# Kernel tuning notes

Hardware: AMD Instinct MI355X
Metric: run time of the kernel (lower is better)

Reference implementation:

```python
import jax, jax.numpy as jnp
import numpy as np
import math

B, S, D, H_HEADS, K_SPAN = 2, 2048, 64, 12, 512  # batch, seq, head dim, heads, pos_ebd_size


def setup_inputs() -> dict:
    key = jax.random.key(0)
    ks = jax.random.split(key, 12)
    init = lambda k, shp: (jax.random.normal(k, shp, dtype=jnp.float32) * 0.02)
    H = jax.random.normal(ks[0], (B, S, D), dtype=jnp.float32)
    pos_embeddings = jax.random.normal(ks[1], (2 * K_SPAN, D), dtype=jnp.float32)
    # classic DeBERTa relative positions: i - j (2-D, as required by the torch code path)
    idx = jnp.arange(S)
    relative_pos = (idx[:, None] - idx[None, :]).astype(jnp.int64)
    OH = H_HEADS * D
    return {
        "H": H,
        "pos_embeddings": pos_embeddings,
        "relative_pos": relative_pos,
        "Wq": init(ks[2], (OH, D)), "bq": jnp.zeros((OH,), jnp.float32),
        "Wk": init(ks[3], (OH, D)), "bk": jnp.zeros((OH,), jnp.float32),
        "Wv": init(ks[4], (OH, D)), "bv": jnp.zeros((OH,), jnp.float32),
        "Wpq": init(ks[5], (OH, D)), "bpq": jnp.zeros((OH,), jnp.float32),
        "Wpk": init(ks[6], (OH, D)), "bpk": jnp.zeros((OH,), jnp.float32),
    }


def _heads(x):
    # [..., S, h*d] -> [..., h, S, d]
    b, s, _ = x.shape
    return x.reshape(b, s, H_HEADS, D).transpose(0, 2, 1, 3)


def reference(H, pos_embeddings, relative_pos, Wq, bq, Wk, bk, Wv, bv, Wpq, bpq, Wpk, bpk):
    proj = lambda x, W, b: x @ W.T + b
    q = _heads(proj(H, Wq, bq))  # [B,h,S,d]
    k = _heads(proj(H, Wk, bk))
    v = _heads(proj(H, Wv, bv))

    # content-to-content scores
    scores = jnp.einsum('bhqd,bhkd->bhqk', q, k)  # [B,h,S,S]

    # relative position projections over the full 2K span
    pk = proj(pos_embeddings, Wpk, bpk).reshape(2 * K_SPAN, H_HEADS, D).transpose(1, 0, 2)  # [h,2K,d]
    pq = proj(pos_embeddings, Wpq, bpq).reshape(2 * K_SPAN, H_HEADS, D).transpose(1, 0, 2)

    rel = relative_pos.astype(jnp.int32)
    # content-to-position: gather over 2K axis with clamped (i-j)+K
    c2p = jnp.einsum('bhqd,hrd->bhqr', q, pk)  # [B,h,S,2K]
    c2p_pos = jnp.clip(rel + K_SPAN, 0, 2 * K_SPAN - 1)  # [S,S]
    c2p_idx = jnp.broadcast_to(c2p_pos[None, None], (B, H_HEADS, S, S))
    c2p_att = jnp.take_along_axis(c2p, c2p_idx, axis=-1)  # [B,h,S,S]

    # position-to-content: gather over 2K axis with clamped -(i-j)+K, then transpose
    p2c = jnp.einsum('bhkd,hrd->bhkr', k, pq)  # [B,h,S,2K]
    p2c_pos = jnp.clip(-rel + K_SPAN, 0, 2 * K_SPAN - 1)
    p2c_idx = jnp.broadcast_to(p2c_pos[None, None], (B, H_HEADS, S, S))
    p2c_att = jnp.take_along_axis(p2c, p2c_idx, axis=-1).swapaxes(-1, -2)  # [B,h,S,S]

    scores = (scores + c2p_att + p2c_att) / math.sqrt(D * 3)
    probs = jax.nn.softmax(scores, axis=-1)
    ctx = jnp.einsum('bhqk,bhkd->bhqd', probs, v)  # [B,h,S,d]
    return ctx.transpose(0, 2, 1, 3).reshape(B, S, H_HEADS * D)
```

## Files before the change

### kernel.cpp

```cpp
#include <hip/hip_runtime.h>
#include <math.h>


#define S_LEN 2048
#define NH    12
#define TWOK  1024
#define QSZ   3145728
#define PSZ   786432
#define POSF  11010048

typedef __bf16 bf16x8 __attribute__((ext_vector_type(8)));
typedef unsigned short u16x8 __attribute__((ext_vector_type(8)));
typedef float f32x4  __attribute__((ext_vector_type(4)));
typedef float f32x16 __attribute__((ext_vector_type(16)));
typedef unsigned int u32x2 __attribute__((ext_vector_type(2)));
typedef unsigned int u32x4 __attribute__((ext_vector_type(4)));

__device__ __forceinline__ unsigned short f2bf(float f) {
  return __builtin_bit_cast(unsigned short, (__bf16)f);
}
__device__ __forceinline__ unsigned pk2bf(float a, float b) {
  return ((unsigned)__builtin_bit_cast(unsigned short, (__bf16)b) << 16)
       | (unsigned)__builtin_bit_cast(unsigned short, (__bf16)a);
}
__device__ __forceinline__ float bf2f(unsigned short h) {
  return __builtin_bit_cast(float, ((unsigned)h) << 16);
}
__device__ __forceinline__ bf16x8 ld_bf8(const unsigned short* p) {
  return __builtin_bit_cast(bf16x8, *(const u16x8*)p);
}

__global__ __launch_bounds__(256) void prep_kernel(
    const float* __restrict__ Hx, const float* __restrict__ pos,
    const float* __restrict__ Wq, const float* __restrict__ Wk,
    const float* __restrict__ Wv, const float* __restrict__ Wpk,
    const float* __restrict__ Wpq,
    const float* __restrict__ bq, const float* __restrict__ bk,
    const float* __restrict__ bv, const float* __restrict__ bpk,
    const float* __restrict__ bpq,
    unsigned short* __restrict__ whi, unsigned short* __restrict__ wlo,
    unsigned short* __restrict__ wall, float* __restrict__ ball) {
  int idx = blockIdx.x * 256 + threadIdx.x;
  if (idx < 327680) {
    float v = (idx < 262144) ? Hx[idx] : pos[idx - 262144];
    __bf16 hi = (__bf16)v;
    float lo = v - (float)hi;
    whi[idx] = __builtin_bit_cast(unsigned short, hi);
    wlo[idx] = f2bf(lo);
  } else if (idx < 573440) {
    int k = idx - 327680;
    int mat = k / 49152, off = k - mat * 49152;
    const float* W = mat==0?Wq: mat==1?Wk: mat==2?Wv: mat==3?Wpk:Wpq;
    wall[k] = f2bf(W[off]);
  } else if (idx < 577280) {
    int k = idx - 573440;
    int mat = k / 768, off = k - mat * 768;
    const float* B = mat==0?bq: mat==1?bk: mat==2?bv: mat==3?bpk:bpq;
    ball[k] = B[off];
  }
}

__global__ __launch_bounds__(256) void proj_gemm(
    const unsigned short* __restrict__ whi, const unsigned short* __restrict__ wlo,
    const unsigned short* __restrict__ wall, const float* __restrict__ ball,
    unsigned short* __restrict__ ws) {
  unsigned short* qg  = ws;
  unsigned short* kg  = ws + QSZ;
  unsigned short* vtg = ws + 2 * QSZ;
  unsigned short* pkg = ws + 3 * QSZ;
  unsigned short* pqg = ws + 3 * QSZ + PSZ;

  int bid = blockIdx.x;
  int rbase, obase, wrow, isA;
  if (bid < 2304) { rbase = (bid / 36) * 64;        obase = (bid % 36) * 64; wrow = obase;        isA = 1; }
  else { int b2 = bid - 2304; rbase = 4096 + (b2 / 24) * 64; obase = (b2 % 24) * 64; wrow = 2304 + obase; isA = 0; }

  int tid = threadIdx.x, w = tid >> 6, l = tid & 63, lg = l >> 4, lr = l & 15;
  int xrow = rbase + w * 16 + lr;

  bf16x8 ah[2], al[2];
  #pragma unroll
  for (int ks = 0; ks < 2; ++ks) {
    ah[ks] = ld_bf8(whi + xrow * 64 + ks * 32 + 8 * lg);
    al[ks] = ld_bf8(wlo + xrow * 64 + ks * 32 + 8 * lg);
  }

  int mat = obase / 768;
  int h = ((obase % 768) >> 6);

  #pragma unroll
  for (int jb = 0; jb < 4; ++jb) {
    f32x4 acc = {0.f, 0.f, 0.f, 0.f};
    #pragma unroll
    for (int ks = 0; ks < 2; ++ks) {
      bf16x8 bfrag = ld_bf8(wall + (wrow + jb * 16 + lr) * 64 + ks * 32 + 8 * lg);
      acc = __builtin_amdgcn_mfma_f32_16x16x32_bf16(ah[ks], bfrag, acc, 0, 0, 0);
      acc = __builtin_amdgcn_mfma_f32_16x16x32_bf16(al[ks], bfrag, acc, 0, 0, 0);
    }
    float bias = ball[wrow + jb * 16 + lr];
    int d = jb * 16 + lr;
    #pragma unroll
    for (int r = 0; r < 4; ++r) {
      int orow = rbase + w * 16 + 4 * lg + r;
      unsigned short val = f2bf(acc[r] + bias);
      if (isA) {
        int bb = orow >> 11, i = orow & 2047, bh = bb * NH + h;
        if (mat == 0)      qg[(bh * S_LEN + i) * 64 + d] = val;
        else if (mat == 1) kg[(bh * S_LEN + i) * 64 + d] = val;
        else               vtg[(bh * 64 + d) * S_LEN + i] = val;
      } else {
        int prow = orow - 4096;
        if (mat == 0) pkg[(h * TWOK + prow) * 64 + d] = val;
        else          pqg[(h * TWOK + prow) * 64 + d] = val;
      }
    }
  }
}

__global__ __launch_bounds__(256) void pos_dots(
    const unsigned short* __restrict__ ws, float* __restrict__ c2p0,
    float* __restrict__ c2p1023, float* __restrict__ p2c0,
    float* __restrict__ p2c1023) {
  int t = blockIdx.x * 256 + threadIdx.x;
  int isK = t >= 49152;
  int row = isK ? t - 49152 : t;
  int h = (row >> 11) % NH;
  const unsigned short* src = ws + (isK ? QSZ : 0) + row * 64;
  const unsigned short* pA = ws + 3 * QSZ + (isK ? PSZ : 0) + (h * TWOK) * 64;
  const unsigned short* pB = pA + 1023 * 64;
  float a0 = 0.f, a1 = 0.f;
  #pragma unroll
  for (int c = 0; c < 8; ++c) {
    u16x8 xv = *(const u16x8*)(src + c * 8);
    u16x8 av = *(const u16x8*)(pA + c * 8);
    u16x8 bv = *(const u16x8*)(pB + c * 8);
    #pragma unroll
    for (int e = 0; e < 8; ++e) {
      float x = bf2f(xv[e]);
      a0 += x * bf2f(av[e]);
      a1 += x * bf2f(bv[e]);
    }
  }
  if (isK) { p2c0[row] = a0; p2c1023[row] = a1; }
  else     { c2p0[row] = a0; c2p1023[row] = a1; }
}

__global__ __launch_bounds__(64, 2) void attn_kernel(
    const unsigned short* __restrict__ ws, float* __restrict__ out) {
  const unsigned short* qg  = ws;
  const unsigned short* kg  = ws + QSZ;
  const unsigned short* vtg = ws + 2 * QSZ;
  const unsigned short* pkg = ws + 3 * QSZ;
  const unsigned short* pqg = ws + 3 * QSZ + PSZ;
  const float* c2p0g    = (const float*)(ws + POSF);
  const float* c2p1023g = c2p0g + 49152;
  const float* p2c0g    = c2p0g + 98304;
  const float* p2c1023g = c2p0g + 147456;

  __shared__ __align__(16) unsigned short tblC[96 * 32];
  __shared__ __align__(16) unsigned short tblP[64 * 128];

  const int bid = blockIdx.x;
  const int g = bid & 7, r = bid >> 3;
  const int bh = 8 * (r % 3) + g;
  const int it32 = r / 3;
  const int b = bh / NH, h = bh - b * NH;
  const int l = threadIdx.x & 63;
  const int iL = l & 31, h5 = l >> 5;
  const int i0w = it32 * 32;
  const int ig = i0w + iL;

  const unsigned short* qb  = qg  + bh * (S_LEN * 64);
  const unsigned short* kb  = kg  + bh * (S_LEN * 64);
  const unsigned short* vb  = vtg + bh * (64 * S_LEN);
  const unsigned short* pkb = pkg + h * (TWOK * 64);
  const unsigned short* pqb = pqg + h * (TWOK * 64);

  const float CS = 1.4426950408889634f / sqrtf(192.0f);

  bf16x8 qf[4];
  #pragma unroll
  for (int kc = 0; kc < 4; ++kc)
    qf[kc] = ld_bf8(qb + ig * 64 + kc * 16 + 8 * h5);

  const float c2pLO = c2p0g[bh * S_LEN + ig];
  const float c2pHI = c2p1023g[bh * S_LEN + ig];

  f32x16 ctx0 = 0.f, ctx1 = 0.f;
  float m_ = -1e30f, l_ = 0.f;

  char* tPw = (char*)tblP;
  char* pb0 = tPw + iL * 256;
  char* pb1 = tPw + (32 + iL) * 256;
  const int wxor = (iL & 15) << 4;

  for (int jt = 0; jt < 32; ++jt) {
    const int j0 = jt * 64;
    const int rlo = 512 + i0w - j0 - 63;
    const int rhi = rlo + 94;

    bf16x8 kf0[4], kf1[4];
    #pragma unroll
    for (int kc = 0; kc < 4; ++kc) {
      kf0[kc] = ld_bf8(kb + (j0 + iL) * 64 + kc * 16 + 8 * h5);
      kf1[kc] = ld_bf8(kb + (j0 + 32 + iL) * 64 + kc * 16 + 8 * h5);
    }
    bf16x8 vf0[4], vf1[4];
    #pragma unroll
    for (int kc = 0; kc < 4; ++kc) {
      vf0[kc] = ld_bf8(vb + (iL) * S_LEN + j0 + kc * 16 + 8 * h5);
      vf1[kc] = ld_bf8(vb + (32 + iL) * S_LEN + j0 + kc * 16 + 8 * h5);
    }

    f32x16 s0 = 0.f, s1 = 0.f;
    #pragma unroll
    for (int kc = 0; kc < 4; ++kc) {
      s0 = __builtin_amdgcn_mfma_f32_32x32x16_bf16(kf0[kc], qf[kc], s0, 0, 0, 0);
      s1 = __builtin_amdgcn_mfma_f32_32x32x16_bf16(kf1[kc], qf[kc], s1, 0, 0, 0);
    }

    if (rlo >= 1023) {
      float pa = p2c1023g[bh * S_LEN + j0 + iL];
      float pb = p2c1023g[bh * S_LEN + j0 + 32 + iL];
      #pragma unroll
      for (int r = 0; r < 16; ++r) {
        const int j32 = (r & 3) + 8 * (r >> 2) + 4 * h5;
        s0[r] = (s0[r] + c2pHI + __shfl(pa, j32)) * CS;
        s1[r] = (s1[r] + c2pHI + __shfl(pb, j32)) * CS;
      }
    } else if (rhi <= 0) {
      float pa = p2c0g[bh * S_LEN + j0 + iL];
      float pb = p2c0g[bh * S_LEN + j0 + 32 + iL];
      #pragma unroll
      for (int r = 0; r < 16; ++r) {
        const int j32 = (r & 3) + 8 * (r >> 2) + 4 * h5;
        s0[r] = (s0[r] + c2pLO + __shfl(pa, j32)) * CS;
        s1[r] = (s1[r] + c2pLO + __shfl(pb, j32)) * CS;
      }
    } else {
      const int rminc = rlo < 0 ? 0 : rlo;
      const int rmaxc = rhi > 1023 ? 1023 : rhi;
      const int bstart = rminc > 928 ? 928 : rminc;
      const int nbh = (rmaxc - bstart) >> 5;
      const int interior = (rlo >= 0) & (rhi <= 1023);
      int c_lo = (rminc - bstart) >> 5;
      int p0_lo, p1_hi;
      if (interior) {
        p0_lo = (rlo + 32 - bstart) >> 5;
        p1_hi = (rhi - 32 - bstart) >> 5;
      } else { p0_lo = c_lo; p1_hi = nbh; }

      for (int nb = c_lo; nb <= nbh; ++nb) {
        const int rrow = bstart + nb * 32 + iL;
        const int doP0 = nb >= p0_lo, doP1 = nb <= p1_hi;
        f32x16 ac = 0.f, a0 = 0.f, a1 = 0.f;
        #pragma unroll
        for (int kc = 0; kc < 4; ++kc) {
          bf16x8 fk = ld_bf8(pkb + rrow * 64 + kc * 16 + 8 * h5);
          ac = __builtin_amdgcn_mfma_f32_32x32x16_bf16(fk, qf[kc], ac, 0, 0, 0);
        }
        if (doP0 | doP1) {
          #pragma unroll
          for (int kc = 0; kc < 4; ++kc) {
            bf16x8 fq = ld_bf8(pqb + rrow * 64 + kc * 16 + 8 * h5);
            if (doP0) a0 = __builtin_amdgcn_mfma_f32_32x32x16_bf16(fq, kf0[kc], a0, 0, 0, 0);
            if (doP1) a1 = __builtin_amdgcn_mfma_f32_32x32x16_bf16(fq, kf1[kc], a1, 0, 0, 0);
          }
        }
        #pragma unroll
        for (int q4 = 0; q4 < 4; ++q4) {
          const int Rq = nb * 32 + 8 * q4 + 4 * h5;
          #pragma unroll
          for (int e = 0; e < 4; ++e)
            tblC[(Rq + e) * 32 + iL] = f2bf(ac[4 * q4 + e]);
        }
        #pragma unroll
        for (int q4 = 0; q4 < 4; ++q4) {
          const int off = ((nb * 32 + 8 * q4 + 4 * h5) * 2) ^ wxor;
          if (doP0) {
            u32x2 v0; v0[0] = pk2bf(a0[4*q4+0], a0[4*q4+1]); v0[1] = pk2bf(a0[4*q4+2], a0[4*q4+3]);
            *(u32x2*)(pb0 + off) = v0;
          }
          if (doP1) {
            u32x2 v1; v1[0] = pk2bf(a1[4*q4+0], a1[4*q4+1]); v1[1] = pk2bf(a1[4*q4+2], a1[4*q4+3]);
            *(u32x2*)(pb1 + off) = v1;
          }
        }
      }
      asm volatile("s_waitcnt lgkmcnt(0)" ::: "memory");

      const int D0 = ig + 512 - j0;
      if (interior) {
        const int rb0 = D0 - bstart;
        #pragma unroll
        for (int r = 0; r < 16; ++r) {
          const int j32 = (r & 3) + 8 * (r >> 2) + 4 * h5;
          const int pxr = (j32 & 15) << 4;
          const int o0 = (rb0 - j32) * 2, o1 = o0 - 64;
          float c0v = bf2f(tblC[(rb0 - j32) * 32 + iL]);
          float c1v = bf2f(tblC[(rb0 - 32 - j32) * 32 + iL]);
          float p0v = bf2f(*(const unsigned short*)(tPw + j32 * 256 + (o0 ^ pxr)));
          float p1v = bf2f(*(const unsigned short*)(tPw + (32 + j32) * 256 + (o1 ^ pxr)));
          s0[r] = (s0[r] + c0v + p0v) * CS;
          s1[r] = (s1[r] + c1v + p1v) * CS;
        }
      } else {
        #pragma unroll
        for (int r = 0; r < 16; ++r) {
          const int j32 = (r & 3) + 8 * (r >> 2) + 4 * h5;
          const int pxr = (j32 & 15) << 4;
          int rel0 = D0 - j32;       rel0 = rel0 < 0 ? 0 : (rel0 > 1023 ? 1023 : rel0);
          int rel1 = D0 - 32 - j32;  rel1 = rel1 < 0 ? 0 : (rel1 > 1023 ? 1023 : rel1);
          const int rb0 = rel0 - bstart, rb1 = rel1 - bstart;
          float c0v = bf2f(tblC[rb0 * 32 + iL]);
          float c1v = bf2f(tblC[rb1 * 32 + iL]);
          float p0v = bf2f(*(const unsigned short*)(tPw + j32 * 256 + ((rb0 * 2) ^ pxr)));
          float p1v = bf2f(*(const unsigned short*)(tPw + (32 + j32) * 256 + ((rb1 * 2) ^ pxr)));
          s0[r] = (s0[r] + c0v + p0v) * CS;
          s1[r] = (s1[r] + c1v + p1v) * CS;
        }
      }
    }

    float vmax = s0[0];
    #pragma unroll
    for (int r = 1; r < 16; ++r) vmax = fmaxf(vmax, s0[r]);
    #pragma unroll
    for (int r = 0; r < 16; ++r) vmax = fmaxf(vmax, s1[r]);
    vmax = fmaxf(vmax, __shfl_xor(vmax, 32));
    float mx = fmaxf(m_, vmax);
    float fs = __builtin_amdgcn_exp2f(m_ - mx);
    m_ = mx;
    float sum = 0.f;
    #pragma unroll
    for (int r = 0; r < 16; ++r) { s0[r] = __builtin_amdgcn_exp2f(s0[r] - mx); sum += s0[r]; }
    #pragma unroll
    for (int r = 0; r < 16; ++r) { s1[r] = __builtin_amdgcn_exp2f(s1[r] - mx); sum += s1[r]; }
    sum += __shfl_xor(sum, 32);
    l_ = l_ * fs + sum;
    if (!__all(fs == 1.0f)) { ctx0 *= fs; ctx1 *= fs; }

    bf16x8 pf[4];
    #pragma unroll
    for (int kc = 0; kc < 4; ++kc) {
      const int c = kc & 1;
      const f32x16& sj = (kc >> 1) ? s1 : s0;
      unsigned X0 = pk2bf(sj[8*c+0], sj[8*c+1]);
      unsigned X1 = pk2bf(sj[8*c+2], sj[8*c+3]);
      unsigned Y0 = pk2bf(sj[8*c+4], sj[8*c+5]);
      unsigned Y1 = pk2bf(sj[8*c+6], sj[8*c+7]);
      unsigned sx0 = (unsigned)__shfl_xor((int)X0, 32);
      unsigned sx1 = (unsigned)__shfl_xor((int)X1, 32);
      unsigned sy0 = (unsigned)__shfl_xor((int)Y0, 32);
      unsigned sy1 = (unsigned)__shfl_xor((int)Y1, 32);
      u32x4 f;
      f[0] = h5 ? sy0 : X0;
      f[1] = h5 ? sy1 : X1;
      f[2] = h5 ? Y0 : sx0;
      f[3] = h5 ? Y1 : sx1;
      pf[kc] = __builtin_bit_cast(bf16x8, f);
    }

    #pragma unroll
    for (int kc = 0; kc < 4; ++kc) {
      ctx0 = __builtin_amdgcn_mfma_f32_32x32x16_bf16(vf0[kc], pf[kc], ctx0, 0, 0, 0);
      ctx1 = __builtin_amdgcn_mfma_f32_32x32x16_bf16(vf1[kc], pf[kc], ctx1, 0, 0, 0);
    }
  }

  float inv = 1.0f / l_;
  float* ob = out + (b * S_LEN + ig) * 768 + h * 64;
  #pragma unroll
  for (int q4 = 0; q4 < 4; ++q4) {
    float4 o0 = {ctx0[4*q4+0]*inv, ctx0[4*q4+1]*inv, ctx0[4*q4+2]*inv, ctx0[4*q4+3]*inv};
    *(float4*)(ob + 8 * q4 + 4 * h5) = o0;
    float4 o1 = {ctx1[4*q4+0]*inv, ctx1[4*q4+1]*inv, ctx1[4*q4+2]*inv, ctx1[4*q4+3]*inv};
    *(float4*)(ob + 32 + 8 * q4 + 4 * h5) = o1;
  }
}

extern "C" void kernel_launch(void* const* d_in, const int* in_sizes, int n_in,
                              void* d_out, int out_size, void* d_ws, size_t ws_size,
                              hipStream_t stream) {
  (void)in_sizes; (void)n_in; (void)out_size; (void)ws_size;
  const float* Hx  = (const float*)d_in[0];
  const float* pos = (const float*)d_in[1];
  const float* Wq  = (const float*)d_in[3];  const float* bq  = (const float*)d_in[4];
  const float* Wk  = (const float*)d_in[5];  const float* bk  = (const float*)d_in[6];
  const float* Wv  = (const float*)d_in[7];  const float* bv  = (const float*)d_in[8];
  const float* Wpq = (const float*)d_in[9];  const float* bpq = (const float*)d_in[10];
  const float* Wpk = (const float*)d_in[11]; const float* bpk = (const float*)d_in[12];
  unsigned short* ws = (unsigned short*)d_ws;

  unsigned short* scratch = (unsigned short*)d_out;
  unsigned short* whi  = scratch;
  unsigned short* wlo  = scratch + 327680;
  unsigned short* wall = scratch + 655360;
  float*          ball = (float*)(scratch + 901120);

  float* c2p0g    = (float*)(ws + POSF);
  float* c2p1023g = c2p0g + 49152;
  float* p2c0g    = c2p0g + 98304;
  float* p2c1023g = c2p0g + 147456;

  prep_kernel<<<2255, 256, 0, stream>>>(Hx, pos, Wq, Wk, Wv, Wpk, Wpq,
                                        bq, bk, bv, bpk, bpq, whi, wlo, wall, ball);
  proj_gemm<<<2688, 256, 0, stream>>>(whi, wlo, wall, ball, ws);
  pos_dots<<<384, 256, 0, stream>>>(ws, c2p0g, c2p1023g, p2c0g, p2c1023g);
  attn_kernel<<<1536, 64, 0, stream>>>(ws, (float*)d_out);
}
```

Measured before the change: 334.4 us.

## Split attention over key blocks, skip unused position bands, vectorize projection stores

The attention kernel gains a split-K (flash-decoding style) mode. Each query tile's key range is split into up to 4 chunks that run as separate blocks and write bf16 partial context plus (m, l). A new combine kernel merges them. The position-band loop now computes only the c2p/p2c bands that actually fall in the tile's diagonal window, and writes them into one packed LDS table. The projection GEMM is re-oriented so outputs are stored as 4-wide vectors instead of scalar 2-byte stores, and launch bounds raise occupancy to 4 waves. The split depends on the workspace size, adds an extra kernel and partial-buffer traffic, and stores partial context in bf16, which costs some precision.

```diff
diff --git a/kernel.cpp b/kernel.cpp
--- a/kernel.cpp
+++ b/kernel.cpp
@@ -11,9 +11,9 @@
 
 typedef __bf16 bf16x8 __attribute__((ext_vector_type(8)));
 typedef unsigned short u16x8 __attribute__((ext_vector_type(8)));
+typedef unsigned short u16x4 __attribute__((ext_vector_type(4)));
 typedef float f32x4  __attribute__((ext_vector_type(4)));
 typedef float f32x16 __attribute__((ext_vector_type(16)));
-typedef unsigned int u32x2 __attribute__((ext_vector_type(2)));
 typedef unsigned int u32x4 __attribute__((ext_vector_type(4)));
 
 __device__ __forceinline__ unsigned short f2bf(float f) {
@@ -76,42 +76,60 @@
   else { int b2 = bid - 2304; rbase = 4096 + (b2 / 24) * 64; obase = (b2 % 24) * 64; wrow = 2304 + obase; isA = 0; }
 
   int tid = threadIdx.x, w = tid >> 6, l = tid & 63, lg = l >> 4, lr = l & 15;
-  int xrow = rbase + w * 16 + lr;
-
-  bf16x8 ah[2], al[2];
+  int mat = obase / 768;
+  int h = (obase % 768) >> 6;
+  int ohrow = wrow + w * 16;
+
+  bf16x8 wf[2];
   #pragma unroll
-  for (int ks = 0; ks < 2; ++ks) {
-    ah[ks] = ld_bf8(whi + xrow * 64 + ks * 32 + 8 * lg);
-    al[ks] = ld_bf8(wlo + xrow * 64 + ks * 32 + 8 * lg);
-  }
-
-  int mat = obase / 768;
-  int h = ((obase % 768) >> 6);
-
-  #pragma unroll
-  for (int jb = 0; jb < 4; ++jb) {
-    f32x4 acc = {0.f, 0.f, 0.f, 0.f};
-    #pragma unroll
-    for (int ks = 0; ks < 2; ++ks) {
-      bf16x8 bfrag = ld_bf8(wall + (wrow + jb * 16 + lr) * 64 + ks * 32 + 8 * lg);
-      acc = __builtin_amdgcn_mfma_f32_16x16x32_bf16(ah[ks], bfrag, acc, 0, 0, 0);
-      acc = __builtin_amdgcn_mfma_f32_16x16x32_bf16(al[ks], bfrag, acc, 0, 0, 0);
-    }
-    float bias = ball[wrow + jb * 16 + lr];
-    int d = jb * 16 + lr;
-    #pragma unroll
-    for (int r = 0; r < 4; ++r) {
-      int orow = rbase + w * 16 + 4 * lg + r;
-      unsigned short val = f2bf(acc[r] + bias);
+  for (int ks = 0; ks < 2; ++ks)
+    wf[ks] = ld_bf8(wall + (ohrow + lr) * 64 + ks * 32 + 8 * lg);
+
+  if (isA && mat == 2) {
+    float bias = ball[ohrow + lr];
+    int d = w * 16 + lr;
+    #pragma unroll
+    for (int tg = 0; tg < 4; ++tg) {
+      f32x4 acc = {0.f, 0.f, 0.f, 0.f};
+      #pragma unroll
+      for (int ks = 0; ks < 2; ++ks) {
+        bf16x8 xh = ld_bf8(whi + (rbase + tg * 16 + lr) * 64 + ks * 32 + 8 * lg);
+        bf16x8 xl = ld_bf8(wlo + (rbase + tg * 16 + lr) * 64 + ks * 32 + 8 * lg);
+        acc = __builtin_amdgcn_mfma_f32_16x16x32_bf16(xh, wf[ks], acc, 0, 0, 0);
+        acc = __builtin_amdgcn_mfma_f32_16x16x32_bf16(xl, wf[ks], acc, 0, 0, 0);
+      }
+      int tok0 = rbase + tg * 16 + 4 * lg;
+      int bb = tok0 >> 11, i0 = tok0 & 2047, bh = bb * NH + h;
+      u16x4 pv;
+      #pragma unroll
+      for (int e = 0; e < 4; ++e) pv[e] = f2bf(acc[e] + bias);
+      *(u16x4*)(vtg + (size_t)(bh * 64 + d) * S_LEN + i0) = pv;
+    }
+  } else {
+    float4 bias4 = *(const float4*)(ball + ohrow + 4 * lg);
+    int d0 = w * 16 + 4 * lg;
+    #pragma unroll
+    for (int tg = 0; tg < 4; ++tg) {
+      f32x4 acc = {0.f, 0.f, 0.f, 0.f};
+      #pragma unroll
+      for (int ks = 0; ks < 2; ++ks) {
+        bf16x8 xh = ld_bf8(whi + (rbase + tg * 16 + lr) * 64 + ks * 32 + 8 * lg);
+        bf16x8 xl = ld_bf8(wlo + (rbase + tg * 16 + lr) * 64 + ks * 32 + 8 * lg);
+        acc = __builtin_amdgcn_mfma_f32_16x16x32_bf16(wf[ks], xh, acc, 0, 0, 0);
+        acc = __builtin_amdgcn_mfma_f32_16x16x32_bf16(wf[ks], xl, acc, 0, 0, 0);
+      }
+      int tok = rbase + tg * 16 + lr;
+      u16x4 pv;
+      pv[0] = f2bf(acc[0] + bias4.x); pv[1] = f2bf(acc[1] + bias4.y);
+      pv[2] = f2bf(acc[2] + bias4.z); pv[3] = f2bf(acc[3] + bias4.w);
       if (isA) {
-        int bb = orow >> 11, i = orow & 2047, bh = bb * NH + h;
-        if (mat == 0)      qg[(bh * S_LEN + i) * 64 + d] = val;
-        else if (mat == 1) kg[(bh * S_LEN + i) * 64 + d] = val;
-        else               vtg[(bh * 64 + d) * S_LEN + i] = val;
+        int bb = tok >> 11, i = tok & 2047, bh = bb * NH + h;
+        unsigned short* dst = (mat == 0 ? qg : kg) + (size_t)(bh * S_LEN + i) * 64 + d0;
+        *(u16x4*)dst = pv;
       } else {
-        int prow = orow - 4096;
-        if (mat == 0) pkg[(h * TWOK + prow) * 64 + d] = val;
-        else          pqg[(h * TWOK + prow) * 64 + d] = val;
+        int prow = tok - 4096;
+        unsigned short* dst = (mat == 0 ? pkg : pqg) + (size_t)(h * TWOK + prow) * 64 + d0;
+        *(u16x4*)dst = pv;
       }
     }
   }
@@ -145,8 +163,10 @@
   else     { c2p0[row] = a0; c2p1023[row] = a1; }
 }
 
-__global__ __launch_bounds__(64, 2) void attn_kernel(
-    const unsigned short* __restrict__ ws, float* __restrict__ out) {
+template<int SPLIT>
+__global__ __launch_bounds__(64, 4) void attn_kernel(
+    const unsigned short* __restrict__ ws, float* __restrict__ out,
+    unsigned short* __restrict__ ctxP, float* __restrict__ mlP) {
   const unsigned short* qg  = ws;
   const unsigned short* kg  = ws + QSZ;
   const unsigned short* vtg = ws + 2 * QSZ;
@@ -157,11 +177,12 @@
   const float* p2c0g    = c2p0g + 98304;
   const float* p2c1023g = c2p0g + 147456;
 
-  __shared__ __align__(16) unsigned short tblC[96 * 32];
-  __shared__ __align__(16) unsigned short tblP[64 * 128];
+  __shared__ unsigned int tbl2[64 * 32];
 
   const int bid = blockIdx.x;
-  const int g = bid & 7, r = bid >> 3;
+  const int g = bid & 7;
+  const int r2 = bid >> 3;
+  const int sk = r2 % SPLIT, r = r2 / SPLIT;
   const int bh = 8 * (r % 3) + g;
   const int it32 = r / 3;
   const int b = bh / NH, h = bh - b * NH;
@@ -189,14 +210,13 @@
   f32x16 ctx0 = 0.f, ctx1 = 0.f;
   float m_ = -1e30f, l_ = 0.f;
 
-  char* tPw = (char*)tblP;
-  char* pb0 = tPw + iL * 256;
-  char* pb1 = tPw + (32 + iL) * 256;
-  const int wxor = (iL & 15) << 4;
-
-  for (int jt = 0; jt < 32; ++jt) {
+  const int jt0 = sk * (32 / SPLIT);
+  const int jt1 = jt0 + (32 / SPLIT);
+
+  for (int jt = jt0; jt < jt1; ++jt) {
     const int j0 = jt * 64;
-    const int rlo = 512 + i0w - j0 - 63;
+    const int D0w = 512 + i0w - j0;
+    const int rlo = D0w - 63;
     const int rhi = rlo + 94;
 
     bf16x8 kf0[4], kf1[4];
@@ -223,119 +243,129 @@
       float pa = p2c1023g[bh * S_LEN + j0 + iL];
       float pb = p2c1023g[bh * S_LEN + j0 + 32 + iL];
       #pragma unroll
-      for (int r = 0; r < 16; ++r) {
-        const int j32 = (r & 3) + 8 * (r >> 2) + 4 * h5;
-        s0[r] = (s0[r] + c2pHI + __shfl(pa, j32)) * CS;
-        s1[r] = (s1[r] + c2pHI + __shfl(pb, j32)) * CS;
+      for (int rr = 0; rr < 16; ++rr) {
+        const int j32 = (rr & 3) + 8 * (rr >> 2) + 4 * h5;
+        s0[rr] = (s0[rr] + c2pHI + __shfl(pa, j32)) * CS;
+        s1[rr] = (s1[rr] + c2pHI + __shfl(pb, j32)) * CS;
       }
     } else if (rhi <= 0) {
       float pa = p2c0g[bh * S_LEN + j0 + iL];
       float pb = p2c0g[bh * S_LEN + j0 + 32 + iL];
       #pragma unroll
-      for (int r = 0; r < 16; ++r) {
-        const int j32 = (r & 3) + 8 * (r >> 2) + 4 * h5;
-        s0[r] = (s0[r] + c2pLO + __shfl(pa, j32)) * CS;
-        s1[r] = (s1[r] + c2pLO + __shfl(pb, j32)) * CS;
+      for (int rr = 0; rr < 16; ++rr) {
+        const int j32 = (rr & 3) + 8 * (rr >> 2) + 4 * h5;
+        s0[rr] = (s0[rr] + c2pLO + __shfl(pa, j32)) * CS;
+        s1[rr] = (s1[rr] + c2pLO + __shfl(pb, j32)) * CS;
       }
     } else {
       const int rminc = rlo < 0 ? 0 : rlo;
       const int rmaxc = rhi > 1023 ? 1023 : rhi;
       const int bstart = rminc > 928 ? 928 : rminc;
-      const int nbh = (rmaxc - bstart) >> 5;
+      const int nbands = ((rmaxc - bstart) >> 5) + 1;
+      const int base = D0w - bstart;
       const int interior = (rlo >= 0) & (rhi <= 1023);
-      int c_lo = (rminc - bstart) >> 5;
-      int p0_lo, p1_hi;
-      if (interior) {
-        p0_lo = (rlo + 32 - bstart) >> 5;
-        p1_hi = (rhi - 32 - bstart) >> 5;
-      } else { p0_lo = c_lo; p1_hi = nbh; }
-
-      for (int nb = c_lo; nb <= nbh; ++nb) {
-        const int rrow = bstart + nb * 32 + iL;
-        const int doP0 = nb >= p0_lo, doP1 = nb <= p1_hi;
-        f32x16 ac = 0.f, a0 = 0.f, a1 = 0.f;
-        #pragma unroll
-        for (int kc = 0; kc < 4; ++kc) {
-          bf16x8 fk = ld_bf8(pkb + rrow * 64 + kc * 16 + 8 * h5);
-          ac = __builtin_amdgcn_mfma_f32_32x32x16_bf16(fk, qf[kc], ac, 0, 0, 0);
+
+      for (int nb = 0; nb < nbands; ++nb) {
+        const int relb0 = nb * 32;
+        const bool needC  = (relb0 <= base + 31) && (relb0 + 31 >= base - 63);
+        const bool needP0 = (relb0 <= base + 31) && (relb0 + 31 >= base - 31);
+        const bool needP1 = (relb0 <= base - 1)  && (relb0 + 31 >= base - 63);
+        const int rrow = bstart + relb0 + iL;
+
+        if (needC) {
+          f32x16 ac = 0.f;
+          #pragma unroll
+          for (int kc = 0; kc < 4; ++kc) {
+            bf16x8 fk = ld_bf8(pkb + rrow * 64 + kc * 16 + 8 * h5);
+            ac = __builtin_amdgcn_mfma_f32_32x32x16_bf16(fk, qf[kc], ac, 0, 0, 0);
+          }
+          #pragma unroll
+          for (int q4 = 0; q4 < 4; ++q4) {
+            #pragma unroll
+            for (int e = 0; e < 4; ++e) {
+              const int relb = relb0 + 8 * q4 + 4 * h5 + e;
+              const int js = base + iL - relb;
+              if (js >= 0 && js < 64)
+                ((unsigned short*)tbl2)[(js * 32 + iL) * 2] = f2bf(ac[4 * q4 + e]);
+            }
+          }
         }
-        if (doP0 | doP1) {
+        if (needP0 | needP1) {
+          f32x16 a0 = 0.f, a1 = 0.f;
           #pragma unroll
           for (int kc = 0; kc < 4; ++kc) {
             bf16x8 fq = ld_bf8(pqb + rrow * 64 + kc * 16 + 8 * h5);
-            if (doP0) a0 = __builtin_amdgcn_mfma_f32_32x32x16_bf16(fq, kf0[kc], a0, 0, 0, 0);
-            if (doP1) a1 = __builtin_amdgcn_mfma_f32_32x32x16_bf16(fq, kf1[kc], a1, 0, 0, 0);
+            if (needP0) a0 = __builtin_amdgcn_mfma_f32_32x32x16_bf16(fq, kf0[kc], a0, 0, 0, 0);
+            if (needP1) a1 = __builtin_amdgcn_mfma_f32_32x32x16_bf16(fq, kf1[kc], a1, 0, 0, 0);
+          }
+          #pragma unroll
+          for (int q4 = 0; q4 < 4; ++q4) {
+            #pragma unroll
+            for (int e = 0; e < 4; ++e) {
+              const int relb = relb0 + 8 * q4 + 4 * h5 + e;
+              if (needP0) {
+                const int i2 = relb + iL - base;
+                if (i2 >= 0 && i2 < 32)
+                  ((unsigned short*)tbl2)[(iL * 32 + i2) * 2 + 1] = f2bf(a0[4 * q4 + e]);
+              }
+              if (needP1) {
+                const int i2 = relb + 32 + iL - base;
+                if (i2 >= 0 && i2 < 32)
+                  ((unsigned short*)tbl2)[((32 + iL) * 32 + i2) * 2 + 1] = f2bf(a1[4 * q4 + e]);
+              }
+            }
           }
         }
+      }
+      asm volatile("s_waitcnt lgkmcnt(0)" ::: "memory");
+
+      if (interior) {
         #pragma unroll
-        for (int q4 = 0; q4 < 4; ++q4) {
-          const int Rq = nb * 32 + 8 * q4 + 4 * h5;
-          #pragma unroll
-          for (int e = 0; e < 4; ++e)
-            tblC[(Rq + e) * 32 + iL] = f2bf(ac[4 * q4 + e]);
-        }
-        #pragma unroll
-        for (int q4 = 0; q4 < 4; ++q4) {
-          const int off = ((nb * 32 + 8 * q4 + 4 * h5) * 2) ^ wxor;
-          if (doP0) {
-            u32x2 v0; v0[0] = pk2bf(a0[4*q4+0], a0[4*q4+1]); v0[1] = pk2bf(a0[4*q4+2], a0[4*q4+3]);
-            *(u32x2*)(pb0 + off) = v0;
-          }
-          if (doP1) {
-            u32x2 v1; v1[0] = pk2bf(a1[4*q4+0], a1[4*q4+1]); v1[1] = pk2bf(a1[4*q4+2], a1[4*q4+3]);
-            *(u32x2*)(pb1 + off) = v1;
-          }
-        }
-      }
-      asm volatile("s_waitcnt lgkmcnt(0)" ::: "memory");
-
-      const int D0 = ig + 512 - j0;
-      if (interior) {
-        const int rb0 = D0 - bstart;
-        #pragma unroll
-        for (int r = 0; r < 16; ++r) {
-          const int j32 = (r & 3) + 8 * (r >> 2) + 4 * h5;
-          const int pxr = (j32 & 15) << 4;
-          const int o0 = (rb0 - j32) * 2, o1 = o0 - 64;
-          float c0v = bf2f(tblC[(rb0 - j32) * 32 + iL]);
-          float c1v = bf2f(tblC[(rb0 - 32 - j32) * 32 + iL]);
-          float p0v = bf2f(*(const unsigned short*)(tPw + j32 * 256 + (o0 ^ pxr)));
-          float p1v = bf2f(*(const unsigned short*)(tPw + (32 + j32) * 256 + (o1 ^ pxr)));
-          s0[r] = (s0[r] + c0v + p0v) * CS;
-          s1[r] = (s1[r] + c1v + p1v) * CS;
+        for (int rr = 0; rr < 16; ++rr) {
+          const int j32 = (rr & 3) + 8 * (rr >> 2) + 4 * h5;
+          const unsigned t0 = tbl2[j32 * 32 + iL];
+          const unsigned t1 = tbl2[(32 + j32) * 32 + iL];
+          s0[rr] = (s0[rr] + bf2f((unsigned short)t0) + bf2f((unsigned short)(t0 >> 16))) * CS;
+          s1[rr] = (s1[rr] + bf2f((unsigned short)t1) + bf2f((unsigned short)(t1 >> 16))) * CS;
         }
       } else {
+        const int D0 = D0w + iL;
+        float paL = p2c0g[bh * S_LEN + j0 + iL];
+        float paH = p2c1023g[bh * S_LEN + j0 + iL];
+        float pbL = p2c0g[bh * S_LEN + j0 + 32 + iL];
+        float pbH = p2c1023g[bh * S_LEN + j0 + 32 + iL];
         #pragma unroll
-        for (int r = 0; r < 16; ++r) {
-          const int j32 = (r & 3) + 8 * (r >> 2) + 4 * h5;
-          const int pxr = (j32 & 15) << 4;
-          int rel0 = D0 - j32;       rel0 = rel0 < 0 ? 0 : (rel0 > 1023 ? 1023 : rel0);
-          int rel1 = D0 - 32 - j32;  rel1 = rel1 < 0 ? 0 : (rel1 > 1023 ? 1023 : rel1);
-          const int rb0 = rel0 - bstart, rb1 = rel1 - bstart;
-          float c0v = bf2f(tblC[rb0 * 32 + iL]);
-          float c1v = bf2f(tblC[rb1 * 32 + iL]);
-          float p0v = bf2f(*(const unsigned short*)(tPw + j32 * 256 + ((rb0 * 2) ^ pxr)));
-          float p1v = bf2f(*(const unsigned short*)(tPw + (32 + j32) * 256 + ((rb1 * 2) ^ pxr)));
-          s0[r] = (s0[r] + c0v + p0v) * CS;
-          s1[r] = (s1[r] + c1v + p1v) * CS;
+        for (int rr = 0; rr < 16; ++rr) {
+          const int j32 = (rr & 3) + 8 * (rr >> 2) + 4 * h5;
+          const int raw0 = D0 - j32, raw1 = D0 - 32 - j32;
+          const unsigned t0 = tbl2[j32 * 32 + iL];
+          const unsigned t1 = tbl2[(32 + j32) * 32 + iL];
+          const float saL = __shfl(paL, j32), saH = __shfl(paH, j32);
+          const float sbL = __shfl(pbL, j32), sbH = __shfl(pbH, j32);
+          float c0 = raw0 <= 0 ? c2pLO : (raw0 >= 1023 ? c2pHI : bf2f((unsigned short)t0));
+          float p0 = raw0 <= 0 ? saL   : (raw0 >= 1023 ? saH   : bf2f((unsigned short)(t0 >> 16)));
+          float c1 = raw1 <= 0 ? c2pLO : (raw1 >= 1023 ? c2pHI : bf2f((unsigned short)t1));
+          float p1 = raw1 <= 0 ? sbL   : (raw1 >= 1023 ? sbH   : bf2f((unsigned short)(t1 >> 16)));
+          s0[rr] = (s0[rr] + c0 + p0) * CS;
+          s1[rr] = (s1[rr] + c1 + p1) * CS;
         }
       }
     }
 
     float vmax = s0[0];
     #pragma unroll
-    for (int r = 1; r < 16; ++r) vmax = fmaxf(vmax, s0[r]);
-    #pragma unroll
-    for (int r = 0; r < 16; ++r) vmax = fmaxf(vmax, s1[r]);
+    for (int rr = 1; rr < 16; ++rr) vmax = fmaxf(vmax, s0[rr]);
+    #pragma unroll
+    for (int rr = 0; rr < 16; ++rr) vmax = fmaxf(vmax, s1[rr]);
     vmax = fmaxf(vmax, __shfl_xor(vmax, 32));
     float mx = fmaxf(m_, vmax);
     float fs = __builtin_amdgcn_exp2f(m_ - mx);
     m_ = mx;
     float sum = 0.f;
     #pragma unroll
-    for (int r = 0; r < 16; ++r) { s0[r] = __builtin_amdgcn_exp2f(s0[r] - mx); sum += s0[r]; }
-    #pragma unroll
-    for (int r = 0; r < 16; ++r) { s1[r] = __builtin_amdgcn_exp2f(s1[r] - mx); sum += s1[r]; }
+    for (int rr = 0; rr < 16; ++rr) { s0[rr] = __builtin_amdgcn_exp2f(s0[rr] - mx); sum += s0[rr]; }
+    #pragma unroll
+    for (int rr = 0; rr < 16; ++rr) { s1[rr] = __builtin_amdgcn_exp2f(s1[rr] - mx); sum += s1[rr]; }
     sum += __shfl_xor(sum, 32);
     l_ = l_ * fs + sum;
     if (!__all(fs == 1.0f)) { ctx0 *= fs; ctx1 *= fs; }
@@ -368,21 +398,68 @@
     }
   }
 
-  float inv = 1.0f / l_;
-  float* ob = out + (b * S_LEN + ig) * 768 + h * 64;
+  if constexpr (SPLIT == 1) {
+    float inv = 1.0f / l_;
+    float* ob = out + (b * S_LEN + ig) * 768 + h * 64;
+    #pragma unroll
+    for (int q4 = 0; q4 < 4; ++q4) {
+      float4 o0 = {ctx0[4*q4+0]*inv, ctx0[4*q4+1]*inv, ctx0[4*q4+2]*inv, ctx0[4*q4+3]*inv};
+      *(float4*)(ob + 8 * q4 + 4 * h5) = o0;
+      float4 o1 = {ctx1[4*q4+0]*inv, ctx1[4*q4+1]*inv, ctx1[4*q4+2]*inv, ctx1[4*q4+3]*inv};
+      *(float4*)(ob + 32 + 8 * q4 + 4 * h5) = o1;
+    }
+  } else {
+    const int rowg = ((bh * 64 + it32) * SPLIT + sk) * 32 + iL;
+    unsigned short* cp = ctxP + (size_t)rowg * 64;
+    #pragma unroll
+    for (int q4 = 0; q4 < 4; ++q4) {
+      u16x4 p0, p1;
+      #pragma unroll
+      for (int e = 0; e < 4; ++e) { p0[e] = f2bf(ctx0[4*q4+e]); p1[e] = f2bf(ctx1[4*q4+e]); }
+      *(u16x4*)(cp + 8 * q4 + 4 * h5) = p0;
+      *(u16x4*)(cp + 32 + 8 * q4 + 4 * h5) = p1;
+    }
+    ((float2*)mlP)[rowg] = make_float2(m_, l_);
+  }
+}
+
+template<int SPLIT>
+__global__ __launch_bounds__(256) void combine_kernel(
+    const unsigned short* __restrict__ ctxP, const float* __restrict__ mlP,
+    float* __restrict__ out) {
+  int t = blockIdx.x * 256 + threadIdx.x;
+  int row = t >> 4, dc = t & 15;
+  int bh = row >> 11, i = row & 2047;
+  int it32 = i >> 5, iL = i & 31;
+  int pbase = ((bh * 64 + it32) * SPLIT) * 32 + iL;
+  float m[SPLIT], lv[SPLIT];
+  float M = -1e30f;
   #pragma unroll
-  for (int q4 = 0; q4 < 4; ++q4) {
-    float4 o0 = {ctx0[4*q4+0]*inv, ctx0[4*q4+1]*inv, ctx0[4*q4+2]*inv, ctx0[4*q4+3]*inv};
-    *(float4*)(ob + 8 * q4 + 4 * h5) = o0;
-    float4 o1 = {ctx1[4*q4+0]*inv, ctx1[4*q4+1]*inv, ctx1[4*q4+2]*inv, ctx1[4*q4+3]*inv};
-    *(float4*)(ob + 32 + 8 * q4 + 4 * h5) = o1;
-  }
+  for (int s = 0; s < SPLIT; ++s) {
+    float2 ml = ((const float2*)mlP)[pbase + s * 32];
+    m[s] = ml.x; lv[s] = ml.y;
+    M = fmaxf(M, ml.x);
+  }
+  float L = 0.f, w[SPLIT];
+  #pragma unroll
+  for (int s = 0; s < SPLIT; ++s) { w[s] = exp2f(m[s] - M); L += lv[s] * w[s]; }
+  float4 o = {0.f, 0.f, 0.f, 0.f};
+  #pragma unroll
+  for (int s = 0; s < SPLIT; ++s) {
+    u16x4 c = *(const u16x4*)(ctxP + (size_t)(pbase + s * 32) * 64 + dc * 4);
+    o.x += bf2f(c[0]) * w[s]; o.y += bf2f(c[1]) * w[s];
+    o.z += bf2f(c[2]) * w[s]; o.w += bf2f(c[3]) * w[s];
+  }
+  float invL = 1.0f / L;
+  int b = bh / NH, h = bh - b * NH;
+  float* op = out + (size_t)(b * S_LEN + i) * 768 + h * 64 + dc * 4;
+  *(float4*)op = make_float4(o.x * invL, o.y * invL, o.z * invL, o.w * invL);
 }
 
 extern "C" void kernel_launch(void* const* d_in, const int* in_sizes, int n_in,
                               void* d_out, int out_size, void* d_ws, size_t ws_size,
                               hipStream_t stream) {
-  (void)in_sizes; (void)n_in; (void)out_size; (void)ws_size;
+  (void)in_sizes; (void)n_in; (void)out_size;
   const float* Hx  = (const float*)d_in[0];
   const float* pos = (const float*)d_in[1];
   const float* Wq  = (const float*)d_in[3];  const float* bq  = (const float*)d_in[4];
@@ -403,9 +480,26 @@
   float* p2c0g    = c2p0g + 98304;
   float* p2c1023g = c2p0g + 147456;
 
+  const size_t base_u16 = POSF + 393216;
+  const size_t unit_bytes = 6684672;
+  int SPLIT = (ws_size >= base_u16 * 2 + 4 * unit_bytes) ? 4
+            : (ws_size >= base_u16 * 2 + 2 * unit_bytes) ? 2 : 1;
+  unsigned short* ctxP = ws + base_u16;
+  float* mlP = (float*)(ctxP + (size_t)SPLIT * 3145728);
+
   prep_kernel<<<2255, 256, 0, stream>>>(Hx, pos, Wq, Wk, Wv, Wpk, Wpq,
                                         bq, bk, bv, bpk, bpq, whi, wlo, wall, ball);
   proj_gemm<<<2688, 256, 0, stream>>>(whi, wlo, wall, ball, ws);
   pos_dots<<<384, 256, 0, stream>>>(ws, c2p0g, c2p1023g, p2c0g, p2c1023g);
-  attn_kernel<<<1536, 64, 0, stream>>>(ws, (float*)d_out);
-}
+
+  float* outf = (float*)d_out;
+  if (SPLIT == 4) {
+    attn_kernel<4><<<1536 * 4, 64, 0, stream>>>(ws, outf, ctxP, mlP);
+    combine_kernel<4><<<3072, 256, 0, stream>>>(ctxP, mlP, outf);
+  } else if (SPLIT == 2) {
+    attn_kernel<2><<<1536 * 2, 64, 0, stream>>>(ws, outf, ctxP, mlP);
+    combine_kernel<2><<<3072, 256, 0, stream>>>(ctxP, mlP, outf);
+  } else {
+    attn_kernel<1><<<1536, 64, 0, stream>>>(ws, outf, ctxP, mlP);
+  }
+}
```

Result: slower. 630.5 us (+88.5%).
